# Optimization experiments

Hardware: AMD Instinct MI355X
Metric: run time of the kernel (lower is better)

The kernel has to match this reference:

```python
import math
import jax, jax.numpy as jnp
import numpy as np

NUM_BINS = 8
TRANS = 8
LEFT, RIGHT = -1.0, 1.0
MIN_W = MIN_H = MIN_D = 1.0e-4


def setup_inputs() -> dict:
    key = jax.random.key(0)
    ks = jax.random.split(key, 8)
    B, D, H, OUT = 524288, 16, 256, TRANS * (3 * NUM_BINS - 1)
    x = jax.random.uniform(ks[0], (B, D), jnp.float32, -0.99, 0.99)
    W0 = jax.random.normal(ks[1], (8, H), jnp.float32) * (1.0 / math.sqrt(8))
    b0 = jnp.zeros((H,), jnp.float32)
    W1 = jax.random.normal(ks[2], (H, H), jnp.float32) * (1.0 / math.sqrt(H))
    b1 = jnp.zeros((H,), jnp.float32)
    Wout = jax.random.normal(ks[3], (H, OUT), jnp.float32) * (0.1 / math.sqrt(H))
    bout = jnp.zeros((OUT,), jnp.float32)
    return {"x": x, "W0": W0, "b0": b0, "W1": W1, "b1": b1, "Wout": Wout, "bout": bout}


def _rq_spline(x, raw_w, raw_h, raw_d):
    # x: [B, T]; raw_w/raw_h: [B, T, K]; raw_d: [B, T, K-1]
    span = RIGHT - LEFT
    const = math.log(math.exp(1.0 - MIN_D) - 1.0)
    widths = jax.nn.softmax(raw_w, axis=-1)
    heights = jax.nn.softmax(raw_h, axis=-1)
    derivs = jax.nn.softplus(raw_d + const) + MIN_D
    widths = span * (MIN_W + (1.0 - MIN_W * NUM_BINS) * widths)
    heights = span * (MIN_H + (1.0 - MIN_H * NUM_BINS) * heights)
    edge_x = LEFT + jnp.pad(jnp.cumsum(widths, axis=-1), ((0, 0), (0, 0), (1, 0)))
    edge_y = LEFT + jnp.pad(jnp.cumsum(heights, axis=-1), ((0, 0), (0, 0), (1, 0)))
    derivs = jnp.pad(derivs, ((0, 0), (0, 0), (1, 1)), constant_values=1.0)
    out_mask = (x <= LEFT + 1e-3) | (x >= RIGHT - 1e-3)
    x_in = jnp.where(out_mask, 0.0, x)
    # searchsorted(right=True) - 1 == count of edges <= x_in, minus 1
    idx = jnp.clip(jnp.sum(edge_x <= x_in[..., None], axis=-1) - 1, 0, NUM_BINS - 1)
    g = lambda a: jnp.take_along_axis(a, idx[..., None], axis=-1)[..., 0]
    xk, yk = g(edge_x), g(edge_y)
    wk, hk = g(widths), g(heights)
    dk, dk1 = g(derivs), g(derivs[..., 1:])
    sk = hk / wk
    eps = (x_in - xk) / wk
    eps_term = eps * (1.0 - eps)
    eps2 = eps * eps
    beta = sk + (dk1 + dk - 2.0 * sk) * eps_term
    alpha = hk * (sk * eps2 + dk * eps_term)
    output = jnp.where(out_mask, x, yk + alpha / beta)
    logdet = (2.0 * jnp.log(sk)
              + jnp.log(dk1 * eps2 + 2.0 * sk * eps_term + dk * (1.0 - eps) ** 2)
              - 2.0 * jnp.log(beta))
    logdet = jnp.where(out_mask, 0.0, logdet)
    return output, logdet


def reference(x, W0, b0, W1, b1, Wout, bout):
    x1 = x[..., :TRANS]   # transformed half (mask == True)
    x2 = x[..., TRANS:]   # conditioning half
    h = jax.nn.relu(x2 @ W0 + b0)
    h = jax.nn.relu(h @ W1 + b1)
    raw = (h @ Wout + bout).reshape(x.shape[0], TRANS, 3 * NUM_BINS - 1)
    raw_w = raw[..., :NUM_BINS]
    raw_h = raw[..., NUM_BINS:2 * NUM_BINS]
    raw_d = raw[..., 2 * NUM_BINS:]
    y1, logdet = _rq_spline(x1, raw_w, raw_h, raw_d)
    out = jnp.concatenate([y1, x2], axis=-1)
    return out, jnp.sum(logdet, axis=-1)
```

## Files before the change

kernel.cpp:

```cpp
#include <hip/hip_runtime.h>
#include <hip/hip_bf16.h>


typedef __bf16 bf16x8 __attribute__((ext_vector_type(8)));
typedef __bf16 bf16x4v __attribute__((ext_vector_type(4)));
typedef float  f32x8 __attribute__((ext_vector_type(8)));
typedef float  f32x4 __attribute__((ext_vector_type(4)));
typedef float  f32x2 __attribute__((ext_vector_type(2)));

#define MFMA16(a,b,c) __builtin_amdgcn_mfma_f32_16x16x32_bf16((a),(b),(c),0,0,0)

#define SW_W1_OFF 8192
#define SW_WO_OFF 73728
#define SW_TOTAL  122880

#define ROWS    64
#define HSTRIDE 264
#define LOG2E   1.44269504f
#define LN2     0.69314718f
#define SPCONST 0.7806568f
#define ZSENT  (-0.00015680f)

__global__ void prep_kernel(const float* __restrict__ W0,
                            const float* __restrict__ W1,
                            const float* __restrict__ Wout,
                            const float* __restrict__ bout,
                            __bf16* __restrict__ sw)
{
  int i = blockIdx.x * 256 + threadIdx.x;
  if (i >= SW_TOTAL + 192) return;
  if (i >= SW_TOTAL){
    int np = i - SW_TOTAL;
    int t = np / 24, p = np % 24;
    float* boutp = (float*)(sw + SW_TOTAL);
    boutp[np] = (p < 23) ? bout[t*23 + p] * LOG2E : 0.f;
    return;
  }
  const float* src; int K, N, NT, li;
  bool wo = false;
  if (i < SW_W1_OFF)      { src = W0;   K = 8;   N = 256; NT = 16; li = i; }
  else if (i < SW_WO_OFF) { src = W1;   K = 256; N = 256; NT = 16; li = i - SW_W1_OFF; }
  else { src = Wout; K = 256; N = 184; NT = 12; li = i - SW_WO_OFF; wo = true; }
  int j    = li & 7;
  int l    = (li >> 3) & 63;
  int rest = li >> 9;
  int nt   = rest % NT;
  int kb   = rest / NT;
  int k = kb * 32 + ((l >> 4) << 3) + j;
  int n = nt * 16 + (l & 15);
  float v;
  if (wo){
    int t = n / 24, p = n % 24;
    v = (p < 23 && k < K) ? Wout[k*184 + t*23 + p] * LOG2E : 0.f;
  } else {
    v = (k < K && n < N) ? src[k * N + n] : 0.f;
  }
  sw[i] = (__bf16)v;
}

__device__ __forceinline__ bf16x4v relu_cvt(f32x4 s){
  const f32x4 z = {0.f, 0.f, 0.f, 0.f};
  s = __builtin_elementwise_max(s, z);
  return __builtin_convertvector(s, bf16x4v);
}

__device__ __forceinline__ f32x4 bias4(const float* p){
  float4 bb = *(const float4*)p;
  f32x4 c; c[0]=bb.x; c[1]=bb.y; c[2]=bb.z; c[3]=bb.w;
  return c;
}

__global__ __launch_bounds__(512, 8)
void fused_kernel(const float* __restrict__ x,
                  const float* __restrict__ b0v,
                  const float* __restrict__ b1v,
                  const __bf16* __restrict__ sw,
                  float* __restrict__ out,
                  int nrows)
{
  __shared__ __align__(16) unsigned char smem[ROWS * HSTRIDE * 2];
  __bf16* hbuf = (__bf16*)smem;
  __bf16* rawb = hbuf;

  const int tid  = threadIdx.x;
  const int wave = tid >> 6;
  const int lane = tid & 63;
  const int quad = lane >> 4;
  const int l16  = lane & 15;
  const int row0 = blockIdx.x * ROWS;

  const __bf16* swW1 = sw + SW_W1_OFF;
  const __bf16* swWo = sw + SW_WO_OFF;
  const float* boutp = (const float*)(sw + SW_TOTAL);

  if (tid < 2*ROWS){
    int r = tid >> 1, hf = tid & 1;
    long g = (long)row0 + r;
    *(float4*)(out + g*16 + 8 + hf*4) = *(const float4*)(x + g*16 + 8 + hf*4);
  }

  {
    const int mq = wave >> 1;
    const int nh = wave & 1;
    bf16x8 bfr[2];
    #pragma unroll
    for (int nt = 0; nt < 2; nt++){
      bf16x8 b = {};
      if (quad == 0){
        const float* xp = x + (long)(row0 + nh*32 + nt*16 + l16)*16 + 8;
        float4 u = *(const float4*)xp;
        float4 v = *(const float4*)(xp + 4);
        f32x8 xf; xf[0]=u.x; xf[1]=u.y; xf[2]=u.z; xf[3]=u.w;
                  xf[4]=v.x; xf[5]=v.y; xf[6]=v.z; xf[7]=v.w;
        b = __builtin_convertvector(xf, bf16x8);
      }
      bfr[nt] = b;
    }
    #pragma unroll
    for (int mi = 0; mi < 4; mi++){
      int mt = mq*4 + mi;
      bf16x8 a = *(const bf16x8*)(sw + (mt*64 + lane)*8);
      f32x4 ci = bias4(b0v + mt*16 + quad*4);
      #pragma unroll
      for (int nt = 0; nt < 2; nt++){
        f32x4 acc = MFMA16(a, bfr[nt], ci);
        *(bf16x4v*)(hbuf + (nh*32 + nt*16 + l16)*HSTRIDE + mt*16 + quad*4) = relu_cvt(acc);
      }
    }
  }
  __syncthreads();

  {
    f32x4 acc[2][4];
    #pragma unroll
    for (int mi = 0; mi < 2; mi++){
      f32x4 ci = bias4(b1v + (wave*2 + mi)*16 + quad*4);
      #pragma unroll
      for (int bt = 0; bt < 4; bt++) acc[mi][bt] = ci;
    }
    #pragma unroll
    for (int kb = 0; kb < 8; kb++){
      bf16x8 hf[4];
      #pragma unroll
      for (int bt = 0; bt < 4; bt++)
        hf[bt] = *(const bf16x8*)(hbuf + (bt*16 + l16)*HSTRIDE + kb*32 + quad*8);
      #pragma unroll
      for (int mi = 0; mi < 2; mi++){
        bf16x8 a = *(const bf16x8*)(swW1 + ((kb*16 + wave*2 + mi)*64 + lane)*8);
        #pragma unroll
        for (int bt = 0; bt < 4; bt++)
          acc[mi][bt] = MFMA16(a, hf[bt], acc[mi][bt]);
      }
    }
    __syncthreads();
    #pragma unroll
    for (int mi = 0; mi < 2; mi++)
      #pragma unroll
      for (int bt = 0; bt < 4; bt++)
        *(bf16x4v*)(hbuf + (bt*16 + l16)*HSTRIDE + (wave*2+mi)*16 + quad*4) =
            relu_cvt(acc[mi][bt]);
  }
  __syncthreads();

  {
    const int nc = wave & 3;
    const int mh = wave >> 2;
    f32x4 acc[2][3];
    #pragma unroll
    for (int mi = 0; mi < 3; mi++){
      f32x4 ci = bias4(boutp + (nc*3+mi)*16 + quad*4);
      #pragma unroll
      for (int bt = 0; bt < 2; bt++) acc[bt][mi] = ci;
    }
    #pragma unroll
    for (int kb = 0; kb < 8; kb++){
      bf16x8 hf[2];
      #pragma unroll
      for (int bt = 0; bt < 2; bt++)
        hf[bt] = *(const bf16x8*)(hbuf + ((mh*2+bt)*16 + l16)*HSTRIDE + kb*32 + quad*8);
      #pragma unroll
      for (int mi = 0; mi < 3; mi++){
        bf16x8 a = *(const bf16x8*)(swWo + ((kb*12 + nc*3 + mi)*64 + lane)*8);
        #pragma unroll
        for (int bt = 0; bt < 2; bt++)
          acc[bt][mi] = MFMA16(a, hf[bt], acc[bt][mi]);
      }
    }
    __syncthreads();
    #pragma unroll
    for (int mi = 0; mi < 3; mi++){
      int mt = nc*3 + mi;
      #pragma unroll
      for (int bt = 0; bt < 2; bt++){
        int row = (mh*2+bt)*16 + l16;
        *(bf16x4v*)(rawb + row*HSTRIDE + mt*16 + quad*4) =
            __builtin_convertvector(acc[bt][mi], bf16x4v);
      }
    }
  }
  __syncthreads();

  float ld;
  {
    int row = tid >> 3;
    int t   = tid & 7;
    long gr = row0 + row;
    float xv = x[gr*16 + t];

    const __bf16* rr = rawb + row*HSTRIDE + t*24;
    bf16x8 v0 = *(const bf16x8*)(rr);
    bf16x8 v1 = *(const bf16x8*)(rr + 8);
    bf16x8 v2 = *(const bf16x8*)(rr + 16);

    f32x2 ewh[8];
    f32x2 sum = {0.f, 0.f};
    #pragma unroll
    for (int i=0;i<8;i++){
      f32x2 e;
      e[0] = __builtin_amdgcn_exp2f((float)v0[i]);
      e[1] = __builtin_amdgcn_exp2f((float)v1[i]);
      ewh[i] = e; sum += e;
    }
    f32x2 scale;
    scale[0] = 1.9984f * __builtin_amdgcn_rcpf(sum[0]);
    scale[1] = 1.9984f * __builtin_amdgcn_rcpf(sum[1]);
    const f32x2 off2 = {2e-4f, 2e-4f};

    bool msk = (xv <= -0.999f) || (xv >= 0.999f);
    float xin = msk ? 0.f : xv;

    f32x2 whi = ewh[0]*scale + off2;
    f32x2 ec; ec[0] = -1.f + whi[0]; ec[1] = -1.f + whi[1];
    f32x2 xyk = {-1.f, -1.f};
    f32x2 whk = whi;
    float zk = ZSENT, zk1 = (float)v2[0];
    #pragma unroll
    for (int i=1;i<8;i++){
      whi = ewh[i]*scale + off2;
      bool le = (ec[0] <= xin);
      xyk = le ? ec : xyk;
      whk = le ? whi : whk;
      zk  = le ? (float)v2[i-1] : zk;
      zk1 = le ? ((i==7) ? ZSENT : (float)v2[i]) : zk1;
      ec += whi;
    }

    float za = zk + SPCONST, zb = zk1 + SPCONST;
    float dk  = (fmaxf(za,0.f) + __builtin_amdgcn_logf(1.f + __builtin_amdgcn_exp2f(-fabsf(za))))*LN2 + 1e-4f;
    float dk1 = (fmaxf(zb,0.f) + __builtin_amdgcn_logf(1.f + __builtin_amdgcn_exp2f(-fabsf(zb))))*LN2 + 1e-4f;

    float rwk = __builtin_amdgcn_rcpf(whk[0]);
    float sk  = whk[1] * rwk;
    float eps = (xin - xyk[0]) * rwk;
    float om  = 1.f - eps;
    float et  = eps * om;
    float e2  = eps * eps;
    float beta  = sk + (dk1 + dk - 2.f*sk) * et;
    float rb    = __builtin_amdgcn_rcpf(beta);
    float alpha = whk[1] * (sk*e2 + dk*et);
    float yv  = msk ? xv : (xyk[1] + alpha * rb);
    float num = dk1*e2 + 2.f*sk*et + dk*om*om;
    float ldv = msk ? 0.f : __builtin_amdgcn_logf(sk*sk*num*rb*rb) * LN2;

    out[gr*16 + t] = yv;
    ld = ldv;
  }

  float s0 = ld;
  #pragma unroll
  for (int m = 1; m < 8; m <<= 1)
    s0 += __shfl_xor(s0, m);
  if ((lane & 7) == 0)
    out[(long)nrows*16 + row0 + (tid >> 3)] = s0;
}

extern "C" void kernel_launch(void* const* d_in, const int* in_sizes, int n_in,
                              void* d_out, int out_size, void* d_ws, size_t ws_size,
                              hipStream_t stream)
{
  const float* x    = (const float*)d_in[0];
  const float* W0   = (const float*)d_in[1];
  const float* b0   = (const float*)d_in[2];
  const float* W1   = (const float*)d_in[3];
  const float* b1   = (const float*)d_in[4];
  const float* Wout = (const float*)d_in[5];
  const float* bout = (const float*)d_in[6];
  float* out = (float*)d_out;
  __bf16* sw = (__bf16*)d_ws;

  int nrows = in_sizes[0] / 16;
  int ntiles = nrows / ROWS;

  prep_kernel<<<(SW_TOTAL + 192 + 255)/256, 256, 0, stream>>>(W0, W1, Wout, bout, sw);
  fused_kernel<<<ntiles, 512, 0, stream>>>(x, b0, b1, sw, out, nrows);
}
```

Before: 241.7 us.

## Double rows per block to 128 with 1024 threads and remap wave work

Doubles the row tile to 128 rows per block, run by 16 waves, and remaps each GEMM stage's wave-to-tile assignment. Each wave now loads a weight fragment and reuses it across more row tiles, so there are fewer blocks and less repeated weight traffic per row. The passthrough copy of the conditioning half is moved into the per-row spline epilogue. Shared memory per block doubles and each block is larger, which may lower occupancy or lengthen the tail.

```diff
diff --git a/kernel.cpp b/kernel.cpp
--- a/kernel.cpp
+++ b/kernel.cpp
@@ -14,7 +14,7 @@
 #define SW_WO_OFF 73728
 #define SW_TOTAL  122880
 
-#define ROWS    64
+#define ROWS    128
 #define HSTRIDE 264
 #define LOG2E   1.44269504f
 #define LN2     0.69314718f
@@ -70,7 +70,7 @@
   return c;
 }
 
-__global__ __launch_bounds__(512, 8)
+__global__ __launch_bounds__(1024, 8)
 void fused_kernel(const float* __restrict__ x,
                   const float* __restrict__ b0v,
                   const float* __restrict__ b1v,
@@ -93,78 +93,64 @@
   const __bf16* swWo = sw + SW_WO_OFF;
   const float* boutp = (const float*)(sw + SW_TOTAL);
 
-  if (tid < 2*ROWS){
-    int r = tid >> 1, hf = tid & 1;
-    long g = (long)row0 + r;
-    *(float4*)(out + g*16 + 8 + hf*4) = *(const float4*)(x + g*16 + 8 + hf*4);
-  }
-
-  {
-    const int mq = wave >> 1;
-    const int nh = wave & 1;
-    bf16x8 bfr[2];
-    #pragma unroll
-    for (int nt = 0; nt < 2; nt++){
+  {
+    const int mt = wave;
+    bf16x8 a = *(const bf16x8*)(sw + (mt*64 + lane)*8);
+    f32x4 ci = bias4(b0v + mt*16 + quad*4);
+    #pragma unroll
+    for (int bt = 0; bt < 8; bt++){
       bf16x8 b = {};
       if (quad == 0){
-        const float* xp = x + (long)(row0 + nh*32 + nt*16 + l16)*16 + 8;
+        const float* xp = x + (long)(row0 + bt*16 + l16)*16 + 8;
         float4 u = *(const float4*)xp;
         float4 v = *(const float4*)(xp + 4);
         f32x8 xf; xf[0]=u.x; xf[1]=u.y; xf[2]=u.z; xf[3]=u.w;
                   xf[4]=v.x; xf[5]=v.y; xf[6]=v.z; xf[7]=v.w;
         b = __builtin_convertvector(xf, bf16x8);
       }
-      bfr[nt] = b;
-    }
-    #pragma unroll
-    for (int mi = 0; mi < 4; mi++){
-      int mt = mq*4 + mi;
-      bf16x8 a = *(const bf16x8*)(sw + (mt*64 + lane)*8);
-      f32x4 ci = bias4(b0v + mt*16 + quad*4);
-      #pragma unroll
-      for (int nt = 0; nt < 2; nt++){
-        f32x4 acc = MFMA16(a, bfr[nt], ci);
-        *(bf16x4v*)(hbuf + (nh*32 + nt*16 + l16)*HSTRIDE + mt*16 + quad*4) = relu_cvt(acc);
-      }
+      f32x4 acc = MFMA16(a, b, ci);
+      *(bf16x4v*)(hbuf + (bt*16 + l16)*HSTRIDE + mt*16 + quad*4) = relu_cvt(acc);
     }
   }
   __syncthreads();
 
   {
+    const int mp = wave >> 1;
+    const int bh = wave & 1;
     f32x4 acc[2][4];
     #pragma unroll
     for (int mi = 0; mi < 2; mi++){
-      f32x4 ci = bias4(b1v + (wave*2 + mi)*16 + quad*4);
-      #pragma unroll
-      for (int bt = 0; bt < 4; bt++) acc[mi][bt] = ci;
+      f32x4 ci = bias4(b1v + (mp*2 + mi)*16 + quad*4);
+      #pragma unroll
+      for (int bi = 0; bi < 4; bi++) acc[mi][bi] = ci;
     }
     #pragma unroll
     for (int kb = 0; kb < 8; kb++){
       bf16x8 hf[4];
       #pragma unroll
-      for (int bt = 0; bt < 4; bt++)
-        hf[bt] = *(const bf16x8*)(hbuf + (bt*16 + l16)*HSTRIDE + kb*32 + quad*8);
+      for (int bi = 0; bi < 4; bi++)
+        hf[bi] = *(const bf16x8*)(hbuf + ((bh*4+bi)*16 + l16)*HSTRIDE + kb*32 + quad*8);
       #pragma unroll
       for (int mi = 0; mi < 2; mi++){
-        bf16x8 a = *(const bf16x8*)(swW1 + ((kb*16 + wave*2 + mi)*64 + lane)*8);
+        bf16x8 a = *(const bf16x8*)(swW1 + ((kb*16 + mp*2 + mi)*64 + lane)*8);
         #pragma unroll
-        for (int bt = 0; bt < 4; bt++)
-          acc[mi][bt] = MFMA16(a, hf[bt], acc[mi][bt]);
+        for (int bi = 0; bi < 4; bi++)
+          acc[mi][bi] = MFMA16(a, hf[bi], acc[mi][bi]);
       }
     }
     __syncthreads();
     #pragma unroll
     for (int mi = 0; mi < 2; mi++)
       #pragma unroll
-      for (int bt = 0; bt < 4; bt++)
-        *(bf16x4v*)(hbuf + (bt*16 + l16)*HSTRIDE + (wave*2+mi)*16 + quad*4) =
-            relu_cvt(acc[mi][bt]);
+      for (int bi = 0; bi < 4; bi++)
+        *(bf16x4v*)(hbuf + ((bh*4+bi)*16 + l16)*HSTRIDE + (mp*2+mi)*16 + quad*4) =
+            relu_cvt(acc[mi][bi]);
   }
   __syncthreads();
 
   {
     const int nc = wave & 3;
-    const int mh = wave >> 2;
+    const int bq = wave >> 2;
     f32x4 acc[2][3];
     #pragma unroll
     for (int mi = 0; mi < 3; mi++){
@@ -177,7 +163,7 @@
       bf16x8 hf[2];
       #pragma unroll
       for (int bt = 0; bt < 2; bt++)
-        hf[bt] = *(const bf16x8*)(hbuf + ((mh*2+bt)*16 + l16)*HSTRIDE + kb*32 + quad*8);
+        hf[bt] = *(const bf16x8*)(hbuf + ((bq*2+bt)*16 + l16)*HSTRIDE + kb*32 + quad*8);
       #pragma unroll
       for (int mi = 0; mi < 3; mi++){
         bf16x8 a = *(const bf16x8*)(swWo + ((kb*12 + nc*3 + mi)*64 + lane)*8);
@@ -192,7 +178,7 @@
       int mt = nc*3 + mi;
       #pragma unroll
       for (int bt = 0; bt < 2; bt++){
-        int row = (mh*2+bt)*16 + l16;
+        int row = (bq*2+bt)*16 + l16;
         *(bf16x4v*)(rawb + row*HSTRIDE + mt*16 + quad*4) =
             __builtin_convertvector(acc[bt][mi], bf16x4v);
       }
@@ -206,6 +192,7 @@
     int t   = tid & 7;
     long gr = row0 + row;
     float xv = x[gr*16 + t];
+    float xpass = x[gr*16 + 8 + t];
 
     const __bf16* rr = rawb + row*HSTRIDE + t*24;
     bf16x8 v0 = *(const bf16x8*)(rr);
@@ -262,7 +249,8 @@
     float num = dk1*e2 + 2.f*sk*et + dk*om*om;
     float ldv = msk ? 0.f : __builtin_amdgcn_logf(sk*sk*num*rb*rb) * LN2;
 
-    out[gr*16 + t] = yv;
+    out[gr*16 + t]     = yv;
+    out[gr*16 + 8 + t] = xpass;
     ld = ldv;
   }
 
@@ -292,5 +280,5 @@
   int ntiles = nrows / ROWS;
 
   prep_kernel<<<(SW_TOTAL + 192 + 255)/256, 256, 0, stream>>>(W0, W1, Wout, bout, sw);
-  fused_kernel<<<ntiles, 512, 0, stream>>>(x, b0, b1, sw, out, nrows);
-}
+  fused_kernel<<<ntiles, 1024, 0, stream>>>(x, b0, b1, sw, out, nrows);
+}
```

Result: slower. 279.1 us (+15.4%).
